# Kernel optimization log

Hardware: AMD Instinct MI355X
Metric: run time of the kernel (lower is better)

The kernel has to match this reference:

```python
import jax, jax.numpy as jnp
import numpy as np

OUT_SL = 32


def gru_cell(x, h, Wih, Whh, bih, bhh):
    # PyTorch GRU cell: gates ordered (r, z, n)
    gi = x @ Wih.T + bih
    gh = h @ Whh.T + bhh
    ir, iz, inn = jnp.split(gi, 3, axis=-1)
    hr, hz, hn = jnp.split(gh, 3, axis=-1)
    r = jax.nn.sigmoid(ir + hr)
    z = jax.nn.sigmoid(iz + hz)
    n = jnp.tanh(inn + r * hn)
    return (1.0 - z) * n + z * h


def run_gru_layer(xs, h0, Wih, Whh, bih, bhh, reverse=False):
    def step(h, x):
        h = gru_cell(x, h, Wih, Whh, bih, bhh)
        return h, h
    hT, ys = jax.lax.scan(step, h0, xs, reverse=reverse)
    return ys, hT


def setup_inputs() -> dict:
    key = jax.random.key(0)
    ks = iter(jax.random.split(key, 32))

    def p(shape, fan_in):
        return (jax.random.normal(next(ks), shape, dtype=jnp.float32)
                / np.sqrt(fan_in).astype(np.float32))

    V_ENC, V_DEC, EE, ED, NH = 32000, 32000, 300, 300, 256
    inp = jax.random.randint(next(ks), (128, 64), 0, V_ENC)
    return {
        'emb_enc': p((V_ENC, EE), 1.0),
        'enc_Wih0': p((2, 3 * NH, EE), EE),
        'enc_Whh0': p((2, 3 * NH, NH), NH),
        'enc_bih0': p((2, 3 * NH), NH),
        'enc_bhh0': p((2, 3 * NH), NH),
        'enc_Wih1': p((2, 3 * NH, 2 * NH), 2 * NH),
        'enc_Whh1': p((2, 3 * NH, NH), NH),
        'enc_bih1': p((2, 3 * NH), NH),
        'enc_bhh1': p((2, 3 * NH), NH),
        'W_out_enc': p((ED, 2 * NH), 2 * NH),
        'emb_dec': p((V_DEC, ED), 1.0),
        'dec_Wih': p((2, 3 * ED, ED), ED),
        'dec_Whh': p((2, 3 * ED, ED), ED),
        'dec_bih': p((2, 3 * ED), ED),
        'dec_bhh': p((2, 3 * ED), ED),
        'W1': p((2 * NH, ED), 2 * NH),
        'l2_W': p((ED, ED), ED),
        'l2_b': p((ED,), ED),
        'l3_W': p((ED, ED + 2 * NH), ED + 2 * NH),
        'l3_b': p((ED,), ED),
        'V_att': p((ED,), ED),
        'out_b': p((V_DEC,), ED),
        'inp': inp,
    }


def reference(emb_enc, enc_Wih0, enc_Whh0, enc_bih0, enc_bhh0,
              enc_Wih1, enc_Whh1, enc_bih1, enc_bhh1, W_out_enc,
              emb_dec, dec_Wih, dec_Whh, dec_bih, dec_bhh,
              W1, l2_W, l2_b, l3_W, l3_b, V_att, out_b, inp):
    sl, bs = inp.shape
    nh = enc_Whh0.shape[-1]
    h0 = jnp.zeros((bs, nh), dtype=emb_enc.dtype)

    # ---- encoder: 2-layer bidirectional GRU (dropout in eval mode = identity)
    emb = emb_enc[inp]                                        # (sl, bs, EE)
    yf0, hf0 = run_gru_layer(emb, h0, enc_Wih0[0], enc_Whh0[0], enc_bih0[0], enc_bhh0[0])
    yb0, hb0 = run_gru_layer(emb, h0, enc_Wih0[1], enc_Whh0[1], enc_bih0[1], enc_bhh0[1], reverse=True)
    x1 = jnp.concatenate([yf0, yb0], axis=-1)                 # (sl, bs, 2*nh)
    yf1, hf1 = run_gru_layer(x1, h0, enc_Wih1[0], enc_Whh1[0], enc_bih1[0], enc_bhh1[0])
    yb1, hb1 = run_gru_layer(x1, h0, enc_Wih1[1], enc_Whh1[1], enc_bih1[1], enc_bhh1[1], reverse=True)
    enc_out = jnp.concatenate([yf1, yb1], axis=-1)            # (sl, bs, 2*nh)

    # h.view(2,2,bs,-1).permute(0,2,1,3) -> concat fwd/bwd per layer
    h = jnp.stack([jnp.concatenate([hf0, hb0], axis=-1),
                   jnp.concatenate([hf1, hb1], axis=-1)])     # (2, bs, 2*nh)
    h = h @ W_out_enc.T                                       # (2, bs, ED)

    w1e = enc_out @ W1                                        # (sl, bs, ED)
    dec_inp0 = jnp.zeros((bs,), dtype=jnp.int32)

    def dec_step(carry, _):
        h, dec_inp = carry
        w2h = h[-1] @ l2_W.T + l2_b                           # (bs, ED)
        u = jnp.tanh(w1e + w2h[None])                         # (sl, bs, ED)
        a = jax.nn.softmax(u @ V_att, axis=0)                 # (sl, bs), softmax over seq
        Xa = jnp.einsum('sb,sbd->bd', a, enc_out)             # (bs, 2*nh)
        e = emb_dec[dec_inp]                                  # (bs, ED)
        x = jnp.concatenate([e, Xa], axis=1) @ l3_W.T + l3_b  # (bs, ED)
        h0n = gru_cell(x, h[0], dec_Wih[0], dec_Whh[0], dec_bih[0], dec_bhh[0])
        h1n = gru_cell(h0n, h[1], dec_Wih[1], dec_Whh[1], dec_bih[1], dec_bhh[1])
        outp = h1n @ emb_dec.T + out_b                        # (bs, V_dec), tied weights
        ndec = jnp.argmax(outp, axis=1).astype(jnp.int32)
        return (jnp.stack([h0n, h1n]), ndec), outp

    (_, _), res = jax.lax.scan(dec_step, (h, dec_inp0), None, length=OUT_SL)
    return res                                                # (out_sl, bs, V_dec)
```

## Files before the change

kernel.cpp:

```cpp
#include <hip/hip_runtime.h>
#include <math.h>


#define DINL static __device__ __forceinline__

DINL float sigm(float x) { return 1.0f / (1.0f + expf(-x)); }
DINL float dot4f(float4 a, float4 b) { return a.x*b.x + a.y*b.y + a.z*b.z + a.w*b.w; }

DINL unsigned long long packmax(float x, int v) {
  unsigned u = __float_as_uint(x);
  u = (u & 0x80000000u) ? ~u : (u | 0x80000000u);
  return ((unsigned long long)u << 32) | (unsigned)(~v);
}
DINL unsigned long long umax64(unsigned long long a, unsigned long long b) {
  return a > b ? a : b;
}

DINL void flagbar(int* flags, int selfid, int n, int target, int tid) {
  __syncthreads();
  if (tid == 0)
    __hip_atomic_store(&flags[selfid * 32], target, __ATOMIC_RELEASE, __HIP_MEMORY_SCOPE_AGENT);
  for (int i = tid; i < n; i += 256) {
    while (__hip_atomic_load(&flags[i * 32], __ATOMIC_ACQUIRE, __HIP_MEMORY_SCOPE_AGENT) < target)
      __builtin_amdgcn_s_sleep(1);
  }
  __syncthreads();
}

__global__ __launch_bounds__(256) void k_embed(const float4* __restrict__ E,
                                               const int* __restrict__ inp,
                                               float4* __restrict__ out) {
  int i = blockIdx.x * 256 + threadIdx.x;
  if (i >= 8192 * 75) return;
  int row = i / 75, q = i - row * 75;
  out[i] = E[(size_t)inp[row] * 75 + q];
}

__global__ __launch_bounds__(256) void k_transpose(const float* __restrict__ A,
                                                   float* __restrict__ B, int R, int C) {
  __shared__ float tile[32][33];
  int c0 = blockIdx.x * 32, r0 = blockIdx.y * 32;
  int tx = threadIdx.x & 31, ty = threadIdx.x >> 5;
  for (int i = 0; i < 32; i += 8) {
    int r = r0 + ty + i, c = c0 + tx;
    if (r < R && c < C) tile[ty + i][tx] = A[(size_t)r * C + c];
  }
  __syncthreads();
  for (int i = 0; i < 32; i += 8) {
    int c = c0 + ty + i, r = r0 + tx;
    if (c < C && r < R) B[(size_t)c * R + r] = tile[tx][ty + i];
  }
}

__global__ __launch_bounds__(256) void k_gemm128(const float* __restrict__ A,
                                                 const float* __restrict__ B,
                                                 const float* __restrict__ bias,
                                                 float* __restrict__ C,
                                                 int N, int M, int K) {
  __shared__ float As[8][132];
  __shared__ float Bs[8][132];
  const int tid = threadIdx.x;
  const int bn = blockIdx.x * 128, bm = blockIdx.y * 128;
  const int tn = (tid >> 4) << 3, tm = (tid & 15) << 3;
  const int r = tid & 127;
  const bool isB = tid >= 128;
  const float* src = isB ? (B + (size_t)(bm + r) * K) : (A + (size_t)(bn + r) * K);
  const bool rowok = isB ? (bm + r < M) : (bn + r < N);
  float acc[8][8] = {};
  for (int k0 = 0; k0 < K; k0 += 8) {
    float v[8];
    if (rowok && k0 + 8 <= K) {
      float4 p0 = *(const float4*)(src + k0);
      float4 p1 = *(const float4*)(src + k0 + 4);
      v[0]=p0.x; v[1]=p0.y; v[2]=p0.z; v[3]=p0.w;
      v[4]=p1.x; v[5]=p1.y; v[6]=p1.z; v[7]=p1.w;
    } else {
#pragma unroll
      for (int j = 0; j < 8; ++j) v[j] = (rowok && k0 + j < K) ? src[k0 + j] : 0.0f;
    }
    float (*dst)[132] = isB ? Bs : As;
#pragma unroll
    for (int j = 0; j < 8; ++j) dst[j][r] = v[j];
    __syncthreads();
#pragma unroll
    for (int kk = 0; kk < 8; ++kk) {
      float a[8], b[8];
      *(float4*)&a[0] = *(const float4*)&As[kk][tn];
      *(float4*)&a[4] = *(const float4*)&As[kk][tn + 4];
      *(float4*)&b[0] = *(const float4*)&Bs[kk][tm];
      *(float4*)&b[4] = *(const float4*)&Bs[kk][tm + 4];
#pragma unroll
      for (int i = 0; i < 8; ++i)
#pragma unroll
        for (int j = 0; j < 8; ++j) acc[i][j] += a[i] * b[j];
    }
    __syncthreads();
  }
#pragma unroll
  for (int i = 0; i < 8; ++i) {
    int row = bn + tn + i;
    if (row >= N) continue;
#pragma unroll
    for (int j = 0; j < 8; ++j) {
      int col = bm + tm + j;
      if (col < M) C[(size_t)row * M + col] = acc[i][j] + (bias ? bias[col] : 0.0f);
    }
  }
}

__global__ __launch_bounds__(256) void k_enc_layer(
    const float* __restrict__ giF, const float* __restrict__ giB,
    const float* __restrict__ Whh,
    const float* __restrict__ bhh,
    float* __restrict__ y,
    float* __restrict__ hbuf,
    int* __restrict__ flags) {
  const int dir = blockIdx.z;
  const int c0 = blockIdx.x << 4;
  const int b0 = blockIdx.y << 3;
  const int tid = threadIdx.x;
  const int cl = tid >> 4;
  const int bl = (tid >> 1) & 7;
  const int ks = tid & 1;
  const float* gi = dir ? giB : giF;
  const float* W = Whh + (size_t)dir * 196608;
  const float* bh = bhh + dir * 768;
  float* hb = hbuf + dir * 16384;
  int* myflags = flags + ((dir << 3) + blockIdx.y) * 16 * 32;

  __shared__ __align__(16) float W0[16][260], W1[16][260], W2[16][260];
  __shared__ __align__(16) float hsh[8][260];

  for (int i = tid; i < 48 * 64; i += 256) {
    int row = i >> 6, q = i & 63;
    int g = row >> 4, rc = row & 15;
    float4 w = ((const float4*)W)[(size_t)(c0 + rc + (g << 8)) * 64 + q];
    float* dst = (g == 0) ? &W0[rc][0] : ((g == 1) ? &W1[rc][0] : &W2[rc][0]);
    *(float4*)&dst[q << 2] = w;
  }
  __syncthreads();

  const int b = b0 + bl, c = c0 + cl;
  const float bhr = bh[c], bhz = bh[256 + c], bhn = bh[512 + c];
  const int kbase = ks << 7;

  {
    const int tt0 = dir ? 127 : 0;
    const float* gp = gi + (size_t)tt0 * 49152 + (size_t)b * 768;
    float gr0 = gp[c], gz0 = gp[256 + c], gn0 = gp[512 + c];
    float gr = gr0, gz = gz0, gn = gn0;

    for (int t = 0; t < 128; ++t) {
      const int pp = t & 1;
      {
        const float* hsrc = hb + pp * 32768 + (b0 << 8);
        int i0 = tid, b1 = i0 >> 6, k1 = i0 & 63;
        int i1 = tid + 256, b2 = i1 >> 6, k2 = i1 & 63;
        float4 h0 = *(const float4*)(hsrc + (b1 << 8) + (k1 << 2));
        float4 h1 = *(const float4*)(hsrc + (b2 << 8) + (k2 << 2));
        *(float4*)&hsh[b1][k1 << 2] = h0;
        *(float4*)&hsh[b2][k2 << 2] = h1;
      }
      __syncthreads();

      float nr = 0.f, nz = 0.f, nn = 0.f;
      if (t < 127) {
        const int tn_ = dir ? 126 - t : t + 1;
        const float* gp2 = gi + (size_t)tn_ * 49152 + (size_t)b * 768;
        nr = gp2[c]; nz = gp2[256 + c]; nn = gp2[512 + c];
      }

      float ar = 0.f, az = 0.f, an = 0.f;
#pragma unroll 8
      for (int kq = 0; kq < 32; ++kq) {
        const int k = kbase + (kq << 2);
        float4 hv = *(const float4*)&hsh[bl][k];
        ar += dot4f(hv, *(const float4*)&W0[cl][k]);
        az += dot4f(hv, *(const float4*)&W1[cl][k]);
        an += dot4f(hv, *(const float4*)&W2[cl][k]);
      }
      ar += __shfl_xor(ar, 1);
      az += __shfl_xor(az, 1);
      an += __shfl_xor(an, 1);

      float rg = sigm(gr + ar + bhr);
      float zg = sigm(gz + az + bhz);
      float ng = tanhf(gn + rg * (an + bhn));
      float hnew = (1.f - zg) * ng + zg * hsh[bl][c];

      if (ks == 0) {
        const int tt = dir ? 127 - t : t;
        hb[(pp ^ 1) * 32768 + (b << 8) + c] = hnew;
        y[(size_t)tt * 32768 + (b << 9) + (dir << 8) + c] = hnew;
      }
      gr = nr; gz = nz; gn = nn;

      if (t < 127) flagbar(myflags, blockIdx.x, 16, t + 1, tid);
    }
  }
}

__global__ __launch_bounds__(256) void k_hcat(const float* __restrict__ x1,
                                              const float* __restrict__ encout,
                                              float* __restrict__ hcat) {
  int i = blockIdx.x * 256 + threadIdx.x;
  int l = i >> 15, r = i & 32767, b = r >> 9, d = r & 511;
  const float* src = l ? encout : x1;
  int ts = (d < 256) ? 127 : 0;
  hcat[i] = src[((size_t)(ts << 6) + b) * 512 + d];
}

DINL void gru_phase(int cb, int tid, const float* __restrict__ xin,
                    const float* __restrict__ hin, float* __restrict__ hout,
                    float* __restrict__ houtT,
                    const float* __restrict__ Wih, const float* __restrict__ Whh,
                    const float* __restrict__ bih, const float* __restrict__ bhh,
                    float* xs, float* hs) {
  const int cchunk = cb % 19, bchunk = cb / 19;
  const int cl = tid & 15, bl = tid >> 4;
  const int c = cchunk * 16 + cl;
  const int b0 = bchunk * 16, bq = b0 + bl;
  for (int i = tid; i < 16 * 75; i += 256) {
    int row = i / 75, q = i - row * 75;
    ((float4*)(xs + row * 300))[q] = ((const float4*)(xin + (size_t)(b0 + row) * 300))[q];
    ((float4*)(hs + row * 300))[q] = ((const float4*)(hin + (size_t)(b0 + row) * 300))[q];
  }
  __syncthreads();
  if (c < 300) {
    float gir = bih[c], giz = bih[300 + c], gin = bih[600 + c];
    float ghr = bhh[c], ghz = bhh[300 + c], ghn = bhh[600 + c];
    const float4* wir = (const float4*)(Wih + (size_t)c * 300);
    const float4* wiz = (const float4*)(Wih + (size_t)(300 + c) * 300);
    const float4* win = (const float4*)(Wih + (size_t)(600 + c) * 300);
    const float4* whr = (const float4*)(Whh + (size_t)c * 300);
    const float4* whz = (const float4*)(Whh + (size_t)(300 + c) * 300);
    const float4* whn = (const float4*)(Whh + (size_t)(600 + c) * 300);
    const float4* xr = (const float4*)(xs + bl * 300);
    const float4* hr = (const float4*)(hs + bl * 300);
    for (int q = 0; q < 75; ++q) {
      float4 xv = xr[q], hv = hr[q];
      gir += dot4f(xv, wir[q]);
      giz += dot4f(xv, wiz[q]);
      gin += dot4f(xv, win[q]);
      ghr += dot4f(hv, whr[q]);
      ghz += dot4f(hv, whz[q]);
      ghn += dot4f(hv, whn[q]);
    }
    float r = sigm(gir + ghr), z = sigm(giz + ghz);
    float n = tanhf(gin + r * ghn);
    float hnew = (1.f - z) * n + z * hs[bl * 300 + c];
    hout[(size_t)bq * 300 + c] = hnew;
    if (houtT) houtT[(size_t)c * 64 + bq] = hnew;
  }
}

__global__ __launch_bounds__(256) void k_dec_step(
    const float* __restrict__ hc, float* __restrict__ hn, float* __restrict__ h1T,
    const float* __restrict__ w1e, const float* __restrict__ encout,
    const float* __restrict__ l2W, const float* __restrict__ l2b,
    const float* __restrict__ l3W, const float* __restrict__ l3b,
    const float* __restrict__ Vatt, const float* __restrict__ embdec,
    const float* __restrict__ dWih, const float* __restrict__ dWhh,
    const float* __restrict__ dbih, const float* __restrict__ dbhh,
    const unsigned long long* __restrict__ prev,
    float* __restrict__ xdec, int* __restrict__ flags, int tstep) {
  const int tid = threadIdx.x, cb = blockIdx.x;
  __shared__ __align__(16) float smem[9600];
  float* h1s = smem;
  float* w2h = smem + 304;
  float* eXa = smem + 608;
  float* aa  = smem + 1424;
  float* red = smem + 1552;
  unsigned long long* redb = (unsigned long long*)(smem + 1680);

  if (cb < 64) {
    const int b = cb;
    const float* h1 = hc + 19200;
    if (tid < 128) {
      unsigned long long m = 0ULL;
      if (prev) {
        m = prev[(size_t)tid * 64 + b];
        if (tid < 122) m = umax64(m, prev[(size_t)(tid + 128) * 64 + b]);
      }
      redb[tid] = m;
    }
    for (int i = tid; i < 300; i += 256) h1s[i] = h1[b * 300 + i];
    __syncthreads();
    for (int s = 64; s > 0; s >>= 1) {
      if (tid < s) redb[tid] = umax64(redb[tid], redb[tid + s]);
      __syncthreads();
    }
    const int ib = prev ? (int)(~(unsigned)(redb[0] & 0xFFFFFFFFULL)) : 0;

    for (int m = tid; m < 300; m += 256) {
      const float4* wr = (const float4*)(l2W + (size_t)m * 300);
      const float4* hr = (const float4*)h1s;
      float acc = l2b[m];
      for (int q = 0; q < 75; ++q) acc += dot4f(wr[q], hr[q]);
      w2h[m] = acc;
    }
    __syncthreads();

    if (tid < 128) {
      const float4* wp = (const float4*)(w1e + ((size_t)(tid << 6) + b) * 300);
      const float4* vp = (const float4*)Vatt;
      const float4* hp = (const float4*)w2h;
      float acc = 0.f;
      for (int q = 0; q < 75; ++q) {
        float4 w = wp[q], h = hp[q], v = vp[q];
        acc += tanhf(w.x + h.x) * v.x + tanhf(w.y + h.y) * v.y +
               tanhf(w.z + h.z) * v.z + tanhf(w.w + h.w) * v.w;
      }
      aa[tid] = acc;
      red[tid] = acc;
    }
    __syncthreads();
    for (int s = 64; s > 0; s >>= 1) {
      if (tid < s) red[tid] = fmaxf(red[tid], red[tid + s]);
      __syncthreads();
    }
    float mx = red[0];
    __syncthreads();
    if (tid < 128) {
      float ex = expf(aa[tid] - mx);
      aa[tid] = ex;
      red[tid] = ex;
    }
    __syncthreads();
    for (int s = 64; s > 0; s >>= 1) {
      if (tid < s) red[tid] += red[tid + s];
      __syncthreads();
    }
    float inv = 1.0f / red[0];
    __syncthreads();
    if (tid < 128) aa[tid] *= inv;
    for (int d = tid; d < 300; d += 256) eXa[d] = embdec[(size_t)ib * 300 + d];
    __syncthreads();

    for (int d = tid; d < 512; d += 256) {
      float acc = 0.f;
      for (int s = 0; s < 128; ++s) acc += aa[s] * encout[((size_t)(s << 6) + b) * 512 + d];
      eXa[300 + d] = acc;
    }
    __syncthreads();

    for (int m = tid; m < 300; m += 256) {
      const float4* wr = (const float4*)(l3W + (size_t)m * 812);
      const float4* xr = (const float4*)eXa;
      float acc = l3b[m];
      for (int q = 0; q < 203; ++q) acc += dot4f(wr[q], xr[q]);
      xdec[b * 300 + m] = acc;
    }
  }

  flagbar(flags, cb, 76, 2 * tstep + 1, tid);
  gru_phase(cb, tid, xdec, hc, hn, nullptr, dWih, dWhh, dbih, dbhh,
            smem, smem + 4800);
  flagbar(flags, cb, 76, 2 * tstep + 2, tid);
  gru_phase(cb, tid, hn, hc + 19200, hn + 19200, h1T,
            dWih + 270000, dWhh + 270000, dbih + 900, dbhh + 900,
            smem, smem + 4800);
}

__global__ __launch_bounds__(256) void k_dec_out(const float* __restrict__ embT,
                                                 const float* __restrict__ h1T,
                                                 const float* __restrict__ outb,
                                                 float* __restrict__ out,
                                                 unsigned long long* __restrict__ bests) {
  const int tid = threadIdx.x;
  const int vt = tid & 127, kh = tid >> 7;
  const int v = blockIdx.x * 128 + vt;
  __shared__ float sacc[128][65];
  float acc[64];
#pragma unroll
  for (int i = 0; i < 64; ++i) acc[i] = 0.f;
  const int kb = kh * 150;
  for (int k = kb; k < kb + 150; ++k) {
    float ev = embT[(size_t)k * 32000 + v];
    const float* h = h1T + k * 64;
#pragma unroll
    for (int i = 0; i < 64; ++i) acc[i] += ev * h[i];
  }
  if (kh) {
#pragma unroll
    for (int i = 0; i < 64; ++i) sacc[vt][i] = acc[i];
  }
  __syncthreads();
  if (!kh) {
    float bo = outb[v];
#pragma unroll
    for (int i = 0; i < 64; ++i) {
      float val = acc[i] + sacc[vt][i] + bo;
      out[(size_t)i * 32000 + v] = val;
      sacc[vt][i] = val;
    }
  }
  __syncthreads();
  if (tid < 64) {
    unsigned long long best = 0ULL;
    const int v0 = blockIdx.x * 128;
    for (int q = 0; q < 128; ++q)
      best = umax64(best, packmax(sacc[q][tid], v0 + q));
    bests[(size_t)blockIdx.x * 64 + tid] = best;
  }
}

extern "C" void kernel_launch(void* const* d_in, const int* in_sizes, int n_in,
                              void* d_out_v, int out_size, void* d_ws, size_t ws_size,
                              hipStream_t stream) {
  (void)in_sizes; (void)n_in; (void)out_size; (void)ws_size;
  const float* emb_enc = (const float*)d_in[0];
  const float* eWih0   = (const float*)d_in[1];
  const float* eWhh0   = (const float*)d_in[2];
  const float* ebih0   = (const float*)d_in[3];
  const float* ebhh0   = (const float*)d_in[4];
  const float* eWih1   = (const float*)d_in[5];
  const float* eWhh1   = (const float*)d_in[6];
  const float* ebih1   = (const float*)d_in[7];
  const float* ebhh1   = (const float*)d_in[8];
  const float* Wout    = (const float*)d_in[9];
  const float* emb_dec = (const float*)d_in[10];
  const float* dWih    = (const float*)d_in[11];
  const float* dWhh    = (const float*)d_in[12];
  const float* dbih    = (const float*)d_in[13];
  const float* dbhh    = (const float*)d_in[14];
  const float* W1      = (const float*)d_in[15];
  const float* l2W     = (const float*)d_in[16];
  const float* l2b     = (const float*)d_in[17];
  const float* l3W     = (const float*)d_in[18];
  const float* l3b     = (const float*)d_in[19];
  const float* Vatt    = (const float*)d_in[20];
  const float* outb    = (const float*)d_in[21];
  const int* inp       = (const int*)d_in[22];
  float* d_out = (float*)d_out_v;

  float* ws = (float*)d_ws;
  size_t off = 0;
  auto take = [&](size_t n) { float* p = ws + off; off += (n + 3) & ~(size_t)3; return p; };
  float* embT   = take((size_t)300 * 32000);
  float* encout = take((size_t)8192 * 512);
  float* w1e    = take((size_t)8192 * 300);
  float* W1T    = take((size_t)300 * 512);
  float* hcat   = take((size_t)128 * 512);
  float* dech   = take((size_t)2 * 2 * 64 * 300);
  float* h1T    = take((size_t)300 * 64);
  float* xdec   = take((size_t)64 * 300);
  float* hbuf   = take((size_t)2 * 2 * 64 * 256);
  unsigned long long* bests = (unsigned long long*)take((size_t)250 * 64 * 2);
  int* flags_enc = (int*)take((size_t)2 * 16 * 16 * 32);
  int* flags_dec = (int*)take((size_t)76 * 32);

  float* emb  = d_out;
  float* gi0f = emb + 2457600;
  float* gi0b = gi0f + 6291456;
  float* x1   = gi0b + 6291456;
  float* gi1f = x1 + 4194304;
  float* gi1b = gi1f + 6291456;

  hipMemsetAsync(flags_enc, 0, (2 * 16 * 16 * 32 + 76 * 32) * sizeof(int), stream);

  k_embed<<<2400, 256, 0, stream>>>((const float4*)emb_enc, inp, (float4*)emb);
  k_transpose<<<dim3(10, 16), 256, 0, stream>>>(W1, W1T, 512, 300);
  k_transpose<<<dim3(10, 1000), 256, 0, stream>>>(emb_dec, embT, 32000, 300);

  k_gemm128<<<dim3(64, 6), 256, 0, stream>>>(emb, eWih0, ebih0, gi0f, 8192, 768, 300);
  k_gemm128<<<dim3(64, 6), 256, 0, stream>>>(emb, eWih0 + 230400, ebih0 + 768, gi0b, 8192, 768, 300);
  hipMemsetAsync(hbuf, 0, 2 * 2 * 64 * 256 * sizeof(float), stream);
  k_enc_layer<<<dim3(16, 8, 2), 256, 0, stream>>>(gi0f, gi0b, eWhh0, ebhh0, x1, hbuf, flags_enc);

  k_gemm128<<<dim3(64, 6), 256, 0, stream>>>(x1, eWih1, ebih1, gi1f, 8192, 768, 512);
  k_gemm128<<<dim3(64, 6), 256, 0, stream>>>(x1, eWih1 + 393216, ebih1 + 768, gi1b, 8192, 768, 512);
  hipMemsetAsync(hbuf, 0, 2 * 2 * 64 * 256 * sizeof(float), stream);
  k_enc_layer<<<dim3(16, 8, 2), 256, 0, stream>>>(gi1f, gi1b, eWhh1, ebhh1, encout, hbuf,
                                                  flags_enc + 8192);

  k_hcat<<<256, 256, 0, stream>>>(x1, encout, hcat);
  k_gemm128<<<dim3(1, 3), 256, 0, stream>>>(hcat, Wout, nullptr, dech, 128, 300, 512);
  k_gemm128<<<dim3(64, 3), 256, 0, stream>>>(encout, W1T, nullptr, w1e, 8192, 300, 512);

  for (int t = 0; t < 32; ++t) {
    int cur = t & 1, nxt = cur ^ 1;
    float* hc = dech + cur * 38400;
    float* hn = dech + nxt * 38400;
    k_dec_step<<<76, 256, 0, stream>>>(hc, hn, h1T, w1e, encout, l2W, l2b, l3W, l3b,
                                       Vatt, emb_dec, dWih, dWhh, dbih, dbhh,
                                       t ? bests : nullptr, xdec, flags_dec, t);
    k_dec_out<<<250, 256, 0, stream>>>(embT, h1T, outb,
                                       d_out + (size_t)t * 2048000, bests);
  }
}
```

Before: 12.83 ms.

## Use per-batch-pair encoder recurrence and a single persistent decoder kernel

The encoder recurrence moves from 256 cooperating workgroups that synchronise through global flags every step to 64 independent workgroups. Each one handles two batch rows, keeps h in LDS, and streams a pre-packed Whh from global memory, so the per-step inter-workgroup barrier is gone. The 64 decoder step/output kernel launches become one persistent 256-workgroup kernel with a cheaper global barrier, and the output projection is rewritten as an LDS-tiled 8x4 register-blocked GEMM. In exchange, every encoder workgroup rereads the whole 768 KB Whh each step with little parallelism, and the persistent kernel assumes all 256 workgroups are co-resident.

```diff
diff --git a/kernel.cpp b/kernel.cpp
--- a/kernel.cpp
+++ b/kernel.cpp
@@ -2,28 +2,46 @@
 #include <math.h>
 
 
+typedef unsigned long long ull;
+typedef float v2f __attribute__((ext_vector_type(2)));
+
 #define DINL static __device__ __forceinline__
 
 DINL float sigm(float x) { return 1.0f / (1.0f + expf(-x)); }
 DINL float dot4f(float4 a, float4 b) { return a.x*b.x + a.y*b.y + a.z*b.z + a.w*b.w; }
 
-DINL unsigned long long packmax(float x, int v) {
+DINL ull packmax(float x, int v) {
   unsigned u = __float_as_uint(x);
   u = (u & 0x80000000u) ? ~u : (u | 0x80000000u);
-  return ((unsigned long long)u << 32) | (unsigned)(~v);
-}
-DINL unsigned long long umax64(unsigned long long a, unsigned long long b) {
-  return a > b ? a : b;
-}
-
-DINL void flagbar(int* flags, int selfid, int n, int target, int tid) {
+  return ((ull)u << 32) | (unsigned)(~v);
+}
+DINL ull umax64(ull a, ull b) { return a > b ? a : b; }
+
+DINL float atl(const float* p) {
+  unsigned u = __hip_atomic_load((const unsigned*)p, __ATOMIC_RELAXED,
+                                 __HIP_MEMORY_SCOPE_AGENT);
+  return __uint_as_float(u);
+}
+DINL void atsf(float* p, float v) {
+  __hip_atomic_exchange((unsigned*)p, __float_as_uint(v), __ATOMIC_RELAXED,
+                        __HIP_MEMORY_SCOPE_AGENT);
+}
+DINL ull atl64(const ull* p) {
+  return __hip_atomic_load(p, __ATOMIC_RELAXED, __HIP_MEMORY_SCOPE_AGENT);
+}
+DINL void ats64(ull* p, ull v) {
+  __hip_atomic_exchange(p, v, __ATOMIC_RELAXED, __HIP_MEMORY_SCOPE_AGENT);
+}
+
+DINL void gbar(unsigned* flags, int wg, unsigned target, int tid) {
+  asm volatile("s_waitcnt vmcnt(0)" ::: "memory");
   __syncthreads();
   if (tid == 0)
-    __hip_atomic_store(&flags[selfid * 32], target, __ATOMIC_RELEASE, __HIP_MEMORY_SCOPE_AGENT);
-  for (int i = tid; i < n; i += 256) {
-    while (__hip_atomic_load(&flags[i * 32], __ATOMIC_ACQUIRE, __HIP_MEMORY_SCOPE_AGENT) < target)
-      __builtin_amdgcn_s_sleep(1);
-  }
+    __hip_atomic_exchange(&flags[wg * 32], target, __ATOMIC_RELAXED,
+                          __HIP_MEMORY_SCOPE_AGENT);
+  while (__hip_atomic_load(&flags[tid * 32], __ATOMIC_RELAXED,
+                           __HIP_MEMORY_SCOPE_AGENT) < target)
+    __builtin_amdgcn_s_sleep(1);
   __syncthreads();
 }
 
@@ -50,6 +68,17 @@
     int c = c0 + ty + i, r = r0 + tx;
     if (c < C && r < R) B[(size_t)c * R + r] = tile[tx][ty + i];
   }
+}
+
+__global__ __launch_bounds__(256) void k_packW(const float* __restrict__ Whh,
+                                               float* __restrict__ W2) {
+  int i = blockIdx.x * 256 + threadIdx.x;
+  if (i >= 196608) return;
+  int d = i / 98304, r = i - d * 98304, kp = r / 768, gc = r - kp * 768;
+  const float* src = Whh + (size_t)d * 196608 + (size_t)gc * 256 + kp * 2;
+  float* dst = W2 + (size_t)i * 2;
+  dst[0] = src[0];
+  dst[1] = src[1];
 }
 
 __global__ __launch_bounds__(256) void k_gemm128(const float* __restrict__ A,
@@ -108,95 +137,68 @@
   }
 }
 
-__global__ __launch_bounds__(256) void k_enc_layer(
+__global__ __launch_bounds__(256) void k_enc_rec(
     const float* __restrict__ giF, const float* __restrict__ giB,
-    const float* __restrict__ Whh,
+    const float* __restrict__ W2,
     const float* __restrict__ bhh,
-    float* __restrict__ y,
-    float* __restrict__ hbuf,
-    int* __restrict__ flags) {
-  const int dir = blockIdx.z;
-  const int c0 = blockIdx.x << 4;
-  const int b0 = blockIdx.y << 3;
-  const int tid = threadIdx.x;
-  const int cl = tid >> 4;
-  const int bl = (tid >> 1) & 7;
-  const int ks = tid & 1;
+    float* __restrict__ y) {
+  const int b0 = blockIdx.x * 2;
+  const int dir = blockIdx.y;
+  const int c = threadIdx.x;
   const float* gi = dir ? giB : giF;
-  const float* W = Whh + (size_t)dir * 196608;
+  const v2f* Wv = (const v2f*)(W2 + (size_t)dir * 196608);
   const float* bh = bhh + dir * 768;
-  float* hb = hbuf + dir * 16384;
-  int* myflags = flags + ((dir << 3) + blockIdx.y) * 16 * 32;
-
-  __shared__ __align__(16) float W0[16][260], W1[16][260], W2[16][260];
-  __shared__ __align__(16) float hsh[8][260];
-
-  for (int i = tid; i < 48 * 64; i += 256) {
-    int row = i >> 6, q = i & 63;
-    int g = row >> 4, rc = row & 15;
-    float4 w = ((const float4*)W)[(size_t)(c0 + rc + (g << 8)) * 64 + q];
-    float* dst = (g == 0) ? &W0[rc][0] : ((g == 1) ? &W1[rc][0] : &W2[rc][0]);
-    *(float4*)&dst[q << 2] = w;
-  }
+
+  __shared__ __align__(16) float hls[2][2][258];
+  for (int i = c; i < 2 * 2 * 258; i += 256) ((float*)hls)[i] = 0.0f;
   __syncthreads();
 
-  const int b = b0 + bl, c = c0 + cl;
   const float bhr = bh[c], bhz = bh[256 + c], bhn = bh[512 + c];
-  const int kbase = ks << 7;
-
-  {
-    const int tt0 = dir ? 127 : 0;
-    const float* gp = gi + (size_t)tt0 * 49152 + (size_t)b * 768;
-    float gr0 = gp[c], gz0 = gp[256 + c], gn0 = gp[512 + c];
-    float gr = gr0, gz = gz0, gn = gn0;
-
-    for (int t = 0; t < 128; ++t) {
-      const int pp = t & 1;
-      {
-        const float* hsrc = hb + pp * 32768 + (b0 << 8);
-        int i0 = tid, b1 = i0 >> 6, k1 = i0 & 63;
-        int i1 = tid + 256, b2 = i1 >> 6, k2 = i1 & 63;
-        float4 h0 = *(const float4*)(hsrc + (b1 << 8) + (k1 << 2));
-        float4 h1 = *(const float4*)(hsrc + (b2 << 8) + (k2 << 2));
-        *(float4*)&hsh[b1][k1 << 2] = h0;
-        *(float4*)&hsh[b2][k2 << 2] = h1;
-      }
-      __syncthreads();
-
-      float nr = 0.f, nz = 0.f, nn = 0.f;
-      if (t < 127) {
-        const int tn_ = dir ? 126 - t : t + 1;
-        const float* gp2 = gi + (size_t)tn_ * 49152 + (size_t)b * 768;
-        nr = gp2[c]; nz = gp2[256 + c]; nn = gp2[512 + c];
-      }
-
-      float ar = 0.f, az = 0.f, an = 0.f;
-#pragma unroll 8
-      for (int kq = 0; kq < 32; ++kq) {
-        const int k = kbase + (kq << 2);
-        float4 hv = *(const float4*)&hsh[bl][k];
-        ar += dot4f(hv, *(const float4*)&W0[cl][k]);
-        az += dot4f(hv, *(const float4*)&W1[cl][k]);
-        an += dot4f(hv, *(const float4*)&W2[cl][k]);
-      }
-      ar += __shfl_xor(ar, 1);
-      az += __shfl_xor(az, 1);
-      an += __shfl_xor(an, 1);
-
-      float rg = sigm(gr + ar + bhr);
-      float zg = sigm(gz + az + bhz);
-      float ng = tanhf(gn + rg * (an + bhn));
-      float hnew = (1.f - zg) * ng + zg * hsh[bl][c];
-
-      if (ks == 0) {
-        const int tt = dir ? 127 - t : t;
-        hb[(pp ^ 1) * 32768 + (b << 8) + c] = hnew;
-        y[(size_t)tt * 32768 + (b << 9) + (dir << 8) + c] = hnew;
-      }
-      gr = nr; gz = nz; gn = nn;
-
-      if (t < 127) flagbar(myflags, blockIdx.x, 16, t + 1, tid);
-    }
+
+  const int tt0 = dir ? 127 : 0;
+  const float* g0p = gi + (size_t)tt0 * 49152 + (size_t)b0 * 768;
+  float g0r = g0p[c], g0z = g0p[256 + c], g0n = g0p[512 + c];
+  float g1r = g0p[768 + c], g1z = g0p[1024 + c], g1n = g0p[1280 + c];
+
+  for (int t = 0; t < 128; ++t) {
+    const int cu = t & 1;
+    float p0r = 0, p0z = 0, p0n = 0, p1r = 0, p1z = 0, p1n = 0;
+    if (t < 127) {
+      const int tn_ = dir ? 126 - t : t + 1;
+      const float* gp = gi + (size_t)tn_ * 49152 + (size_t)b0 * 768;
+      p0r = gp[c]; p0z = gp[256 + c]; p0n = gp[512 + c];
+      p1r = gp[768 + c]; p1z = gp[1024 + c]; p1n = gp[1280 + c];
+    }
+    v2f a0r = {0,0}, a0z = {0,0}, a0n = {0,0};
+    v2f a1r = {0,0}, a1z = {0,0}, a1n = {0,0};
+    const float* h0p = &hls[cu][0][0];
+    const float* h1p = &hls[cu][1][0];
+#pragma unroll 4
+    for (int kp = 0; kp < 128; ++kp) {
+      v2f wr = Wv[kp * 768 + c];
+      v2f wz = Wv[kp * 768 + 256 + c];
+      v2f wn = Wv[kp * 768 + 512 + c];
+      v2f h0 = *(const v2f*)&h0p[kp * 2];
+      v2f h1 = *(const v2f*)&h1p[kp * 2];
+      a0r += h0 * wr; a0z += h0 * wz; a0n += h0 * wn;
+      a1r += h1 * wr; a1z += h1 * wz; a1n += h1 * wn;
+    }
+    float r0 = sigm(g0r + a0r.x + a0r.y + bhr);
+    float z0 = sigm(g0z + a0z.x + a0z.y + bhz);
+    float n0 = tanhf(g0n + r0 * (a0n.x + a0n.y + bhn));
+    float h0new = (1.f - z0) * n0 + z0 * h0p[c];
+    float r1 = sigm(g1r + a1r.x + a1r.y + bhr);
+    float z1 = sigm(g1z + a1z.x + a1z.y + bhz);
+    float n1 = tanhf(g1n + r1 * (a1n.x + a1n.y + bhn));
+    float h1new = (1.f - z1) * n1 + z1 * h1p[c];
+    hls[cu ^ 1][0][c] = h0new;
+    hls[cu ^ 1][1][c] = h1new;
+    const int tw = dir ? 127 - t : t;
+    float* yp = y + (size_t)tw * 32768 + (size_t)b0 * 512 + dir * 256 + c;
+    yp[0] = h0new;
+    yp[512] = h1new;
+    g0r = p0r; g0z = p0z; g0n = p0n; g1r = p1r; g1z = p1z; g1n = p1n;
+    __syncthreads();
   }
 }
 
@@ -210,20 +212,20 @@
   hcat[i] = src[((size_t)(ts << 6) + b) * 512 + d];
 }
 
-DINL void gru_phase(int cb, int tid, const float* __restrict__ xin,
-                    const float* __restrict__ hin, float* __restrict__ hout,
-                    float* __restrict__ houtT,
-                    const float* __restrict__ Wih, const float* __restrict__ Whh,
-                    const float* __restrict__ bih, const float* __restrict__ bhh,
-                    float* xs, float* hs) {
+DINL void gru_at(int cb, int tid, const float* __restrict__ xin,
+                 const float* __restrict__ hin, float* __restrict__ hout,
+                 float* __restrict__ houtT,
+                 const float* __restrict__ Wih, const float* __restrict__ Whh,
+                 const float* __restrict__ bih, const float* __restrict__ bhh,
+                 float* xs, float* hs) {
   const int cchunk = cb % 19, bchunk = cb / 19;
   const int cl = tid & 15, bl = tid >> 4;
   const int c = cchunk * 16 + cl;
   const int b0 = bchunk * 16, bq = b0 + bl;
-  for (int i = tid; i < 16 * 75; i += 256) {
-    int row = i / 75, q = i - row * 75;
-    ((float4*)(xs + row * 300))[q] = ((const float4*)(xin + (size_t)(b0 + row) * 300))[q];
-    ((float4*)(hs + row * 300))[q] = ((const float4*)(hin + (size_t)(b0 + row) * 300))[q];
+  for (int i = tid; i < 4800; i += 256) {
+    int row = i / 300, q = i - row * 300;
+    xs[i] = atl(xin + (size_t)(b0 + row) * 300 + q);
+    hs[i] = atl(hin + (size_t)(b0 + row) * 300 + q);
   }
   __syncthreads();
   if (c < 300) {
@@ -249,159 +251,182 @@
     float r = sigm(gir + ghr), z = sigm(giz + ghz);
     float n = tanhf(gin + r * ghn);
     float hnew = (1.f - z) * n + z * hs[bl * 300 + c];
-    hout[(size_t)bq * 300 + c] = hnew;
-    if (houtT) houtT[(size_t)c * 64 + bq] = hnew;
-  }
-}
-
-__global__ __launch_bounds__(256) void k_dec_step(
-    const float* __restrict__ hc, float* __restrict__ hn, float* __restrict__ h1T,
+    atsf(&hout[(size_t)bq * 300 + c], hnew);
+    if (houtT) atsf(&houtT[(size_t)c * 64 + bq], hnew);
+  }
+}
+
+__global__ __launch_bounds__(256) void k_dec_all(
+    float* __restrict__ dech, float* __restrict__ h1T, float* __restrict__ xdec,
+    ull* __restrict__ bests, unsigned* __restrict__ flags,
     const float* __restrict__ w1e, const float* __restrict__ encout,
     const float* __restrict__ l2W, const float* __restrict__ l2b,
     const float* __restrict__ l3W, const float* __restrict__ l3b,
     const float* __restrict__ Vatt, const float* __restrict__ embdec,
     const float* __restrict__ dWih, const float* __restrict__ dWhh,
     const float* __restrict__ dbih, const float* __restrict__ dbhh,
-    const unsigned long long* __restrict__ prev,
-    float* __restrict__ xdec, int* __restrict__ flags, int tstep) {
-  const int tid = threadIdx.x, cb = blockIdx.x;
-  __shared__ __align__(16) float smem[9600];
-  float* h1s = smem;
-  float* w2h = smem + 304;
-  float* eXa = smem + 608;
-  float* aa  = smem + 1424;
-  float* red = smem + 1552;
-  unsigned long long* redb = (unsigned long long*)(smem + 1680);
-
-  if (cb < 64) {
-    const int b = cb;
-    const float* h1 = hc + 19200;
-    if (tid < 128) {
-      unsigned long long m = 0ULL;
-      if (prev) {
-        m = prev[(size_t)tid * 64 + b];
-        if (tid < 122) m = umax64(m, prev[(size_t)(tid + 128) * 64 + b]);
-      }
-      redb[tid] = m;
-    }
-    for (int i = tid; i < 300; i += 256) h1s[i] = h1[b * 300 + i];
-    __syncthreads();
-    for (int s = 64; s > 0; s >>= 1) {
-      if (tid < s) redb[tid] = umax64(redb[tid], redb[tid + s]);
-      __syncthreads();
-    }
-    const int ib = prev ? (int)(~(unsigned)(redb[0] & 0xFFFFFFFFULL)) : 0;
-
-    for (int m = tid; m < 300; m += 256) {
-      const float4* wr = (const float4*)(l2W + (size_t)m * 300);
-      const float4* hr = (const float4*)h1s;
-      float acc = l2b[m];
-      for (int q = 0; q < 75; ++q) acc += dot4f(wr[q], hr[q]);
-      w2h[m] = acc;
-    }
-    __syncthreads();
-
-    if (tid < 128) {
-      const float4* wp = (const float4*)(w1e + ((size_t)(tid << 6) + b) * 300);
-      const float4* vp = (const float4*)Vatt;
-      const float4* hp = (const float4*)w2h;
-      float acc = 0.f;
-      for (int q = 0; q < 75; ++q) {
-        float4 w = wp[q], h = hp[q], v = vp[q];
-        acc += tanhf(w.x + h.x) * v.x + tanhf(w.y + h.y) * v.y +
-               tanhf(w.z + h.z) * v.z + tanhf(w.w + h.w) * v.w;
-      }
-      aa[tid] = acc;
-      red[tid] = acc;
-    }
-    __syncthreads();
-    for (int s = 64; s > 0; s >>= 1) {
-      if (tid < s) red[tid] = fmaxf(red[tid], red[tid + s]);
-      __syncthreads();
-    }
-    float mx = red[0];
-    __syncthreads();
-    if (tid < 128) {
-      float ex = expf(aa[tid] - mx);
-      aa[tid] = ex;
-      red[tid] = ex;
-    }
-    __syncthreads();
-    for (int s = 64; s > 0; s >>= 1) {
-      if (tid < s) red[tid] += red[tid + s];
-      __syncthreads();
-    }
-    float inv = 1.0f / red[0];
-    __syncthreads();
-    if (tid < 128) aa[tid] *= inv;
-    for (int d = tid; d < 300; d += 256) eXa[d] = embdec[(size_t)ib * 300 + d];
-    __syncthreads();
-
-    for (int d = tid; d < 512; d += 256) {
-      float acc = 0.f;
-      for (int s = 0; s < 128; ++s) acc += aa[s] * encout[((size_t)(s << 6) + b) * 512 + d];
-      eXa[300 + d] = acc;
-    }
-    __syncthreads();
-
-    for (int m = tid; m < 300; m += 256) {
-      const float4* wr = (const float4*)(l3W + (size_t)m * 812);
-      const float4* xr = (const float4*)eXa;
-      float acc = l3b[m];
-      for (int q = 0; q < 203; ++q) acc += dot4f(wr[q], xr[q]);
-      xdec[b * 300 + m] = acc;
-    }
-  }
-
-  flagbar(flags, cb, 76, 2 * tstep + 1, tid);
-  gru_phase(cb, tid, xdec, hc, hn, nullptr, dWih, dWhh, dbih, dbhh,
-            smem, smem + 4800);
-  flagbar(flags, cb, 76, 2 * tstep + 2, tid);
-  gru_phase(cb, tid, hn, hc + 19200, hn + 19200, h1T,
-            dWih + 270000, dWhh + 270000, dbih + 900, dbhh + 900,
-            smem, smem + 4800);
-}
-
-__global__ __launch_bounds__(256) void k_dec_out(const float* __restrict__ embT,
-                                                 const float* __restrict__ h1T,
-                                                 const float* __restrict__ outb,
-                                                 float* __restrict__ out,
-                                                 unsigned long long* __restrict__ bests) {
-  const int tid = threadIdx.x;
-  const int vt = tid & 127, kh = tid >> 7;
-  const int v = blockIdx.x * 128 + vt;
-  __shared__ float sacc[128][65];
-  float acc[64];
-#pragma unroll
-  for (int i = 0; i < 64; ++i) acc[i] = 0.f;
-  const int kb = kh * 150;
-  for (int k = kb; k < kb + 150; ++k) {
-    float ev = embT[(size_t)k * 32000 + v];
-    const float* h = h1T + k * 64;
-#pragma unroll
-    for (int i = 0; i < 64; ++i) acc[i] += ev * h[i];
-  }
-  if (kh) {
-#pragma unroll
-    for (int i = 0; i < 64; ++i) sacc[vt][i] = acc[i];
-  }
-  __syncthreads();
-  if (!kh) {
-    float bo = outb[v];
-#pragma unroll
-    for (int i = 0; i < 64; ++i) {
-      float val = acc[i] + sacc[vt][i] + bo;
-      out[(size_t)i * 32000 + v] = val;
-      sacc[vt][i] = val;
-    }
-  }
-  __syncthreads();
-  if (tid < 64) {
-    unsigned long long best = 0ULL;
-    const int v0 = blockIdx.x * 128;
-    for (int q = 0; q < 128; ++q)
-      best = umax64(best, packmax(sacc[q][tid], v0 + q));
-    bests[(size_t)blockIdx.x * 64 + tid] = best;
+    const float* __restrict__ embT, const float* __restrict__ outb,
+    float* __restrict__ out) {
+  const int wg = blockIdx.x, tid = threadIdx.x;
+  __shared__ __align__(16) float smem[14400];
+  unsigned tgt = 0;
+
+  for (int t = 0; t < 32; ++t) {
+    const int cur = t & 1;
+    float* hc = dech + cur * 38400;
+    float* hn = dech + (cur ^ 1) * 38400;
+
+    if (wg < 64) {
+      const int b = wg;
+      float* h1s = smem;
+      float* w2h = smem + 304;
+      float* eXa = smem + 608;
+      float* aa  = smem + 1424;
+      float* red = smem + 1552;
+      ull* redb  = (ull*)(smem + 1680);
+
+      redb[tid] = (t > 0 && tid < 250) ? atl64(&bests[(size_t)tid * 64 + b]) : 0ULL;
+      for (int i = tid; i < 300; i += 256) h1s[i] = atl(hc + 19200 + b * 300 + i);
+      __syncthreads();
+      for (int s = 128; s > 0; s >>= 1) {
+        if (tid < s) redb[tid] = umax64(redb[tid], redb[tid + s]);
+        __syncthreads();
+      }
+      const int ib = (t > 0) ? (int)(~(unsigned)(redb[0] & 0xFFFFFFFFULL)) : 0;
+
+      for (int m = tid; m < 300; m += 256) {
+        const float4* wr = (const float4*)(l2W + (size_t)m * 300);
+        const float4* hr = (const float4*)h1s;
+        float acc = l2b[m];
+        for (int q = 0; q < 75; ++q) acc += dot4f(wr[q], hr[q]);
+        w2h[m] = acc;
+      }
+      __syncthreads();
+
+      if (tid < 128) {
+        const float4* wp = (const float4*)(w1e + ((size_t)(tid << 6) + b) * 300);
+        const float4* vp = (const float4*)Vatt;
+        const float4* hp = (const float4*)w2h;
+        float acc = 0.f;
+        for (int q = 0; q < 75; ++q) {
+          float4 w = wp[q], h = hp[q], v = vp[q];
+          acc += tanhf(w.x + h.x) * v.x + tanhf(w.y + h.y) * v.y +
+                 tanhf(w.z + h.z) * v.z + tanhf(w.w + h.w) * v.w;
+        }
+        aa[tid] = acc;
+        red[tid] = acc;
+      }
+      __syncthreads();
+      for (int s = 64; s > 0; s >>= 1) {
+        if (tid < s) red[tid] = fmaxf(red[tid], red[tid + s]);
+        __syncthreads();
+      }
+      float mx = red[0];
+      __syncthreads();
+      if (tid < 128) {
+        float ex = expf(aa[tid] - mx);
+        aa[tid] = ex;
+        red[tid] = ex;
+      }
+      __syncthreads();
+      for (int s = 64; s > 0; s >>= 1) {
+        if (tid < s) red[tid] += red[tid + s];
+        __syncthreads();
+      }
+      float inv = 1.0f / red[0];
+      __syncthreads();
+      if (tid < 128) aa[tid] *= inv;
+      for (int d = tid; d < 300; d += 256) eXa[d] = embdec[(size_t)ib * 300 + d];
+      __syncthreads();
+
+      for (int d = tid; d < 512; d += 256) {
+        float acc = 0.f;
+        for (int s = 0; s < 128; ++s)
+          acc += aa[s] * encout[((size_t)(s << 6) + b) * 512 + d];
+        eXa[300 + d] = acc;
+      }
+      __syncthreads();
+
+      for (int m = tid; m < 300; m += 256) {
+        const float4* wr = (const float4*)(l3W + (size_t)m * 812);
+        const float4* xr = (const float4*)eXa;
+        float acc = l3b[m];
+        for (int q = 0; q < 203; ++q) acc += dot4f(wr[q], xr[q]);
+        atsf(&xdec[b * 300 + m], acc);
+      }
+    }
+    gbar(flags, wg, ++tgt, tid);
+
+    if (wg < 76)
+      gru_at(wg, tid, xdec, hc, hn, nullptr, dWih, dWhh, dbih, dbhh,
+             smem, smem + 4800);
+    gbar(flags, wg, ++tgt, tid);
+
+    if (wg < 76)
+      gru_at(wg, tid, hn, hc + 19200, hn + 19200, h1T,
+             dWih + 270000, dWhh + 270000, dbih + 900, dbhh + 900,
+             smem, smem + 4800);
+    gbar(flags, wg, ++tgt, tid);
+
+    if (wg < 250) {
+      const int v0 = wg * 128;
+      const int vq = tid & 31, bo = tid >> 5;
+      float acc[8][4];
+#pragma unroll
+      for (int i = 0; i < 8; ++i)
+#pragma unroll
+        for (int j = 0; j < 4; ++j) acc[i][j] = 0.f;
+      float* hch = smem;
+      float* et  = smem + 4800;
+      for (int kc = 0; kc < 4; ++kc) {
+        __syncthreads();
+        for (int i = tid; i < 4800; i += 256) hch[i] = atl(h1T + kc * 4800 + i);
+        for (int i = tid; i < 2400; i += 256) {
+          int row = i >> 5, c4 = (i & 31) << 2;
+          *(float4*)&et[(row << 7) + c4] =
+              *(const float4*)(embT + (size_t)(kc * 75 + row) * 32000 + v0 + c4);
+        }
+        __syncthreads();
+        for (int k = 0; k < 75; ++k) {
+          float hv[8];
+          *(float4*)&hv[0] = *(const float4*)&hch[(k << 6) + (bo << 3)];
+          *(float4*)&hv[4] = *(const float4*)&hch[(k << 6) + (bo << 3) + 4];
+          float4 ev = *(const float4*)&et[(k << 7) + (vq << 2)];
+#pragma unroll
+          for (int i = 0; i < 8; ++i) {
+            acc[i][0] += hv[i] * ev.x;
+            acc[i][1] += hv[i] * ev.y;
+            acc[i][2] += hv[i] * ev.z;
+            acc[i][3] += hv[i] * ev.w;
+          }
+        }
+      }
+      float4 bo4 = *(const float4*)(outb + v0 + (vq << 2));
+      float* outp = out + (size_t)t * 2048000;
+      float* sacc = smem;
+      __syncthreads();
+#pragma unroll
+      for (int i = 0; i < 8; ++i) {
+        const int b = (bo << 3) + i;
+        float4 r;
+        r.x = acc[i][0] + bo4.x; r.y = acc[i][1] + bo4.y;
+        r.z = acc[i][2] + bo4.z; r.w = acc[i][3] + bo4.w;
+        *(float4*)(outp + (size_t)b * 32000 + v0 + (vq << 2)) = r;
+        sacc[((vq << 2) + 0) * 64 + b] = r.x;
+        sacc[((vq << 2) + 1) * 64 + b] = r.y;
+        sacc[((vq << 2) + 2) * 64 + b] = r.z;
+        sacc[((vq << 2) + 3) * 64 + b] = r.w;
+      }
+      __syncthreads();
+      if (tid < 64) {
+        ull best = 0ULL;
+#pragma unroll 4
+        for (int v = 0; v < 128; ++v)
+          best = umax64(best, packmax(sacc[v * 64 + tid], v0 + v));
+        ats64(&bests[(size_t)wg * 64 + tid], best);
+      }
+    }
+    if (t < 31) gbar(flags, wg, ++tgt, tid);
   }
 }
 
@@ -445,10 +470,8 @@
   float* dech   = take((size_t)2 * 2 * 64 * 300);
   float* h1T    = take((size_t)300 * 64);
   float* xdec   = take((size_t)64 * 300);
-  float* hbuf   = take((size_t)2 * 2 * 64 * 256);
-  unsigned long long* bests = (unsigned long long*)take((size_t)250 * 64 * 2);
-  int* flags_enc = (int*)take((size_t)2 * 16 * 16 * 32);
-  int* flags_dec = (int*)take((size_t)76 * 32);
+  ull* bests    = (ull*)take((size_t)250 * 64 * 2);
+  unsigned* flags = (unsigned*)take((size_t)256 * 32);
 
   float* emb  = d_out;
   float* gi0f = emb + 2457600;
@@ -456,36 +479,31 @@
   float* x1   = gi0b + 6291456;
   float* gi1f = x1 + 4194304;
   float* gi1b = gi1f + 6291456;
-
-  hipMemsetAsync(flags_enc, 0, (2 * 16 * 16 * 32 + 76 * 32) * sizeof(int), stream);
+  float* W2L0 = d_out + 33554432;
+  float* W2L1 = W2L0 + 393216;
+
+  hipMemsetAsync(flags, 0, 256 * 32 * sizeof(unsigned), stream);
 
   k_embed<<<2400, 256, 0, stream>>>((const float4*)emb_enc, inp, (float4*)emb);
   k_transpose<<<dim3(10, 16), 256, 0, stream>>>(W1, W1T, 512, 300);
   k_transpose<<<dim3(10, 1000), 256, 0, stream>>>(emb_dec, embT, 32000, 300);
+  k_packW<<<768, 256, 0, stream>>>(eWhh0, W2L0);
+  k_packW<<<768, 256, 0, stream>>>(eWhh1, W2L1);
 
   k_gemm128<<<dim3(64, 6), 256, 0, stream>>>(emb, eWih0, ebih0, gi0f, 8192, 768, 300);
   k_gemm128<<<dim3(64, 6), 256, 0, stream>>>(emb, eWih0 + 230400, ebih0 + 768, gi0b, 8192, 768, 300);
-  hipMemsetAsync(hbuf, 0, 2 * 2 * 64 * 256 * sizeof(float), stream);
-  k_enc_layer<<<dim3(16, 8, 2), 256, 0, stream>>>(gi0f, gi0b, eWhh0, ebhh0, x1, hbuf, flags_enc);
+  k_enc_rec<<<dim3(32, 2), 256, 0, stream>>>(gi0f, gi0b, W2L0, ebhh0, x1);
 
   k_gemm128<<<dim3(64, 6), 256, 0, stream>>>(x1, eWih1, ebih1, gi1f, 8192, 768, 512);
   k_gemm128<<<dim3(64, 6), 256, 0, stream>>>(x1, eWih1 + 393216, ebih1 + 768, gi1b, 8192, 768, 512);
-  hipMemsetAsync(hbuf, 0, 2 * 2 * 64 * 256 * sizeof(float), stream);
-  k_enc_layer<<<dim3(16, 8, 2), 256, 0, stream>>>(gi1f, gi1b, eWhh1, ebhh1, encout, hbuf,
-                                                  flags_enc + 8192);
+  k_enc_rec<<<dim3(32, 2), 256, 0, stream>>>(gi1f, gi1b, W2L1, ebhh1, encout);
 
   k_hcat<<<256, 256, 0, stream>>>(x1, encout, hcat);
   k_gemm128<<<dim3(1, 3), 256, 0, stream>>>(hcat, Wout, nullptr, dech, 128, 300, 512);
   k_gemm128<<<dim3(64, 3), 256, 0, stream>>>(encout, W1T, nullptr, w1e, 8192, 300, 512);
 
-  for (int t = 0; t < 32; ++t) {
-    int cur = t & 1, nxt = cur ^ 1;
-    float* hc = dech + cur * 38400;
-    float* hn = dech + nxt * 38400;
-    k_dec_step<<<76, 256, 0, stream>>>(hc, hn, h1T, w1e, encout, l2W, l2b, l3W, l3b,
-                                       Vatt, emb_dec, dWih, dWhh, dbih, dbhh,
-                                       t ? bests : nullptr, xdec, flags_dec, t);
-    k_dec_out<<<250, 256, 0, stream>>>(embT, h1T, outb,
-                                       d_out + (size_t)t * 2048000, bests);
-  }
-}
+  k_dec_all<<<256, 256, 0, stream>>>(dech, h1T, xdec, bests, flags,
+                                     w1e, encout, l2W, l2b, l3W, l3b,
+                                     Vatt, emb_dec, dWih, dWhh, dbih, dbhh,
+                                     embT, outb, d_out);
+}
```

New measurement: 11.03 ms. 14.0% less time.
